# Kernel tuning notes

Hardware: AMD Instinct MI355X
Metric: run time of the kernel (lower is better)

The kernel has to match this reference:

```python
import jax, jax.numpy as jnp
import numpy as np

N_ATOMS = 16384
N_EDGES = 65536
ATOM_DIM = 29
BOND_DIM = 8
UNITS = 64          # message_units / embed_dim
STEPS = 4
HEADS = 8
DENSE = 512
B_MOL = 256         # molecules
T_ATOMS = 64        # atoms per molecule (N_ATOMS = B_MOL * T_ATOMS)


def setup_inputs() -> dict:
    key = jax.random.key(0)
    ks = jax.random.split(key, 24)
    D = UNITS

    atom_features = jax.random.normal(ks[0], (N_ATOMS, ATOM_DIM), jnp.float32)
    bond_features = jax.random.normal(ks[1], (N_EDGES, BOND_DIM), jnp.float32)
    # edges within molecules
    mol = jax.random.randint(ks[2], (N_EDGES,), 0, B_MOL)
    a = jax.random.randint(ks[3], (N_EDGES,), 0, T_ATOMS)
    b = jax.random.randint(ks[4], (N_EDGES,), 0, T_ATOMS)
    pair_indices = jnp.stack([mol * T_ATOMS + a, mol * T_ATOMS + b], axis=1).astype(jnp.int32)
    molecule_indicator = (jnp.arange(N_ATOMS) // T_ATOMS).astype(jnp.int32)

    def xavier(k, shape, fan_in):
        return jax.random.normal(k, shape, jnp.float32) * (1.0 / np.sqrt(fan_in))

    params = dict(
        kernel=xavier(ks[5], (BOND_DIM, D * D), BOND_DIM),
        kernel_bias=jnp.zeros((D * D,), jnp.float32),
        gru_w_ih=xavier(ks[6], (3 * D, D), D),
        gru_w_hh=xavier(ks[7], (3 * D, D), D),
        gru_b_ih=jnp.zeros((3 * D,), jnp.float32),
        gru_b_hh=jnp.zeros((3 * D,), jnp.float32),
        in_proj_w=xavier(ks[8], (3 * D, D), D),
        in_proj_b=jnp.zeros((3 * D,), jnp.float32),
        out_proj_w=xavier(ks[9], (D, D), D),
        out_proj_b=jnp.zeros((D,), jnp.float32),
        ffn_w1=xavier(ks[10], (D, DENSE), D),
        ffn_b1=jnp.zeros((DENSE,), jnp.float32),
        ffn_w2=xavier(ks[11], (DENSE, D), DENSE),
        ffn_b2=jnp.zeros((D,), jnp.float32),
        ln1_g=jnp.ones((D,), jnp.float32),
        ln1_b=jnp.zeros((D,), jnp.float32),
        ln2_g=jnp.ones((D,), jnp.float32),
        ln2_b=jnp.zeros((D,), jnp.float32),
        d1_w=xavier(ks[12], (D, DENSE), D),
        d1_b=jnp.zeros((DENSE,), jnp.float32),
        d2_w=xavier(ks[13], (DENSE, 1), DENSE),
        d2_b=jnp.zeros((1,), jnp.float32),
    )
    return dict(atom_features=atom_features, bond_features=bond_features,
                pair_indices=pair_indices, molecule_indicator=molecule_indicator, **params)


def _layernorm(x, g, b, eps=1e-5):
    mu = x.mean(-1, keepdims=True)
    var = ((x - mu) ** 2).mean(-1, keepdims=True)
    return (x - mu) * jax.lax.rsqrt(var + eps) * g + b


def _forward(atom_features, bond_features, pair_indices, molecule_indicator,
             kernel, kernel_bias, gru_w_ih, gru_w_hh, gru_b_ih, gru_b_hh,
             in_proj_w, in_proj_b, out_proj_w, out_proj_b,
             ffn_w1, ffn_b1, ffn_w2, ffn_b2, ln1_g, ln1_b, ln2_g, ln2_b,
             d1_w, d1_b, d2_w, d2_b):
    D = UNITS
    n = atom_features.shape[0]
    # pad atom features to message_units
    h = jnp.pad(atom_features, ((0, 0), (0, D - atom_features.shape[1])))

    src = pair_indices[:, 0]
    dst = pair_indices[:, 1]
    # per-edge bond-conditioned transform matrices: [E, D, D]
    bond_mat = (bond_features @ kernel + kernel_bias).reshape(-1, D, D)

    for _ in range(STEPS):
        nbr = h[dst]                                      # gather [E, D]
        msg = jnp.einsum('eij,ej->ei', bond_mat, nbr)     # per-edge matvec
        agg = jax.ops.segment_sum(msg, src, num_segments=n)  # scatter-add [N, D]
        # GRUCell(input=agg, hidden=h)
        gi = agg @ gru_w_ih.T + gru_b_ih
        gh = h @ gru_w_hh.T + gru_b_hh
        i_r, i_z, i_n = jnp.split(gi, 3, axis=-1)
        h_r, h_z, h_n = jnp.split(gh, 3, axis=-1)
        r = jax.nn.sigmoid(i_r + h_r)
        z = jax.nn.sigmoid(i_z + h_z)
        nn_ = jnp.tanh(i_n + r * h_n)
        h = (1.0 - z) * nn_ + z * h

    # PartitionPadding: scatter atoms into [B_MOL, T_ATOMS, D] (indicator sorted, contiguous)
    starts = jnp.searchsorted(molecule_indicator, jnp.arange(B_MOL, dtype=molecule_indicator.dtype))
    pos = jnp.arange(n) - starts[molecule_indicator]
    x = jnp.zeros((B_MOL, T_ATOMS, D), h.dtype).at[molecule_indicator, pos].set(h)

    valid = jnp.any(x != 0, axis=-1)                      # [B, T] key-padding mask

    # multi-head self-attention
    qkv = x @ in_proj_w.T + in_proj_b                     # [B, T, 3D]
    q, k, v = jnp.split(qkv, 3, axis=-1)
    hd = D // HEADS
    q = q.reshape(B_MOL, T_ATOMS, HEADS, hd)
    k = k.reshape(B_MOL, T_ATOMS, HEADS, hd)
    v = v.reshape(B_MOL, T_ATOMS, HEADS, hd)
    scores = jnp.einsum('bqhd,bkhd->bhqk', q, k) / np.sqrt(hd)
    scores = jnp.where(valid[:, None, None, :], scores, -1e9)
    attn = jax.nn.softmax(scores, axis=-1)
    ao = jnp.einsum('bhqk,bkhd->bqhd', attn, v).reshape(B_MOL, T_ATOMS, D)
    ao = ao @ out_proj_w.T + out_proj_b

    y1 = _layernorm(x + ao, ln1_g, ln1_b)
    ffn = jax.nn.relu(y1 @ ffn_w1 + ffn_b1) @ ffn_w2 + ffn_b2
    y2 = _layernorm(y1 + ffn, ln2_g, ln2_b)
    pooled = y2.mean(axis=1)                              # [B, D]

    out = jax.nn.relu(pooled @ d1_w + d1_b)
    return jax.nn.sigmoid(out @ d2_w + d2_b)              # [B, 1]


def reference(atom_features, bond_features, pair_indices, molecule_indicator,
              kernel, kernel_bias, gru_w_ih, gru_w_hh, gru_b_ih, gru_b_hh,
              in_proj_w, in_proj_b, out_proj_w, out_proj_b,
              ffn_w1, ffn_b1, ffn_w2, ffn_b2, ln1_g, ln1_b, ln2_g, ln2_b,
              d1_w, d1_b, d2_w, d2_b):
    return _forward(atom_features, bond_features, pair_indices, molecule_indicator,
                    kernel, kernel_bias, gru_w_ih, gru_w_hh, gru_b_ih, gru_b_hh,
                    in_proj_w, in_proj_b, out_proj_w, out_proj_b,
                    ffn_w1, ffn_b1, ffn_w2, ffn_b2, ln1_g, ln1_b, ln2_g, ln2_b,
                    d1_w, d1_b, d2_w, d2_b)
```

## Files before the change

kernel.cpp:

```cpp
#include <hip/hip_runtime.h>
#include <hip/hip_bf16.h>
#include <math.h>

#define NA 16384
#define NE 65536
#define AD 29

typedef __attribute__((ext_vector_type(8))) short bfrag8;
typedef __attribute__((ext_vector_type(4))) float f32x4;

__device__ __forceinline__ float sigmoidf_(float x) { return 1.0f / (1.0f + expf(-x)); }
__device__ __forceinline__ unsigned short bf16bits(float x) {
  __hip_bfloat16 hb = __float2bfloat16(x);
  return *reinterpret_cast<unsigned short*>(&hb);
}
__device__ __forceinline__ float bf16val(unsigned short u) {
  unsigned int b = ((unsigned int)u) << 16;
  return __uint_as_float(b);
}

__global__ void k_init_h(const float* __restrict__ af, float* __restrict__ h,
                         int* __restrict__ count) {
  int idx = blockIdx.x * 256 + threadIdx.x;
  if (idx >= NA * 64) return;
  if (idx < NA) count[idx] = 0;
  int a = idx >> 6, d = idx & 63;
  h[idx] = (d < AD) ? af[a * AD + d] : 0.0f;
}

__global__ void k_prep_all(
    const float* __restrict__ kern, const float* __restrict__ kbias,
    const float* __restrict__ wih, const float* __restrict__ whh,
    const float* __restrict__ w1, const float* __restrict__ w2,
    const float* __restrict__ ipw, const float* __restrict__ opw,
    unsigned short* __restrict__ KrA,
    unsigned short* __restrict__ Wh, unsigned short* __restrict__ Wl,
    unsigned short* __restrict__ W1h, unsigned short* __restrict__ W1l,
    unsigned short* __restrict__ W2h, unsigned short* __restrict__ W2l,
    unsigned short* __restrict__ PQh, unsigned short* __restrict__ PQl,
    unsigned short* __restrict__ POh, unsigned short* __restrict__ POl) {
  int idx0 = blockIdx.x * 256 + threadIdx.x;
  if (idx0 < 36864) {
    int idx = idx0;
    int r = idx & 7;
    int lane = (idx >> 3) & 63;
    int tmp2 = idx >> 9;
    int ks = tmp2 % 18, w = tmp2 / 18;
    int i = w * 16 + (lane & 15);
    int kj = ks * 32 + ((lane >> 4) << 3) + r;
    int k9 = kj >> 6, j = kj & 63;
    float v = (k9 < 8) ? kern[k9 * 4096 + i * 64 + j] : kbias[i * 64 + j];
    KrA[idx] = bf16bits(v);
  } else if (idx0 < 61440) {
    int idx = idx0 - 36864;
    int r = idx & 7;
    int lane = (idx >> 3) & 63;
    int t2 = idx >> 9;
    int ks = t2 & 1;
    int t3 = t2 >> 1;
    int q = t3 % 6, w = t3 / 6;
    int s = q / 3, g = q % 3;
    int R = g * 64 + w * 16 + (lane & 15);
    int kk = ks * 32 + ((lane >> 4) << 3) + r;
    float v = (s == 0) ? wih[R * 64 + kk] : whh[R * 64 + kk];
    unsigned short hi = bf16bits(v);
    Wh[idx] = hi;
    Wl[idx] = bf16bits(v - bf16val(hi));
  } else if (idx0 < 126976) {
    int idx = idx0 - 61440;
    int r = idx & 7;
    int lane = (idx >> 3) & 63;
    int rest = (idx >> 9) & 63;
    if (idx < 32768) {
      int tile = rest >> 1, ks = rest & 1;
      int hid = tile * 16 + (lane & 15);
      int kk = ks * 32 + ((lane >> 4) << 3) + r;
      float v = w1[kk * 512 + hid];
      unsigned short hi = bf16bits(v);
      W1h[idx] = hi;
      W1l[idx] = bf16bits(v - bf16val(hi));
    } else {
      int i2 = idx - 32768;
      int tile = rest >> 4, ks = rest & 15;
      int outr = tile * 16 + (lane & 15);
      int kk = ks * 32 + ((lane >> 4) << 3) + r;
      float v = w2[kk * 64 + outr];
      unsigned short hi = bf16bits(v);
      W2h[i2] = hi;
      W2l[i2] = bf16bits(v - bf16val(hi));
    }
  } else if (idx0 < 143360) {
    int i = idx0 - 126976;
    if (i < 12288) {
      int r = i & 7;
      int lane = (i >> 3) & 63;
      int rest = i >> 9;
      int t = rest >> 1, ks = rest & 1;
      int R = t * 16 + (lane & 15);
      int kk = ks * 32 + ((lane >> 4) << 3) + r;
      float v = ipw[R * 64 + kk];
      unsigned short hi = bf16bits(v);
      PQh[i] = hi;
      PQl[i] = bf16bits(v - bf16val(hi));
    } else {
      int i2 = i - 12288;
      int r = i2 & 7;
      int lane = (i2 >> 3) & 63;
      int rest = i2 >> 9;
      int t = rest >> 1, ks = rest & 1;
      int R = t * 16 + (lane & 15);
      int kk = ks * 32 + ((lane >> 4) << 3) + r;
      float v = opw[R * 64 + kk];
      unsigned short hi = bf16bits(v);
      POh[i2] = hi;
      POl[i2] = bf16bits(v - bf16val(hi));
    }
  }
}

__global__ void k_count(const int* __restrict__ pairs, int* __restrict__ count) {
  int e = blockIdx.x * 256 + threadIdx.x;
  if (e >= NE) return;
  atomicAdd(&count[pairs[2 * e]], 1);
}
__global__ void k_scan1(const int* __restrict__ count, int* __restrict__ bsum) {
  __shared__ int red[256];
  int b = blockIdx.x, t = threadIdx.x;
  red[t] = count[b * 256 + t];
  __syncthreads();
  for (int s = 128; s > 0; s >>= 1) { if (t < s) red[t] += red[t + s]; __syncthreads(); }
  if (t == 0) bsum[b] = red[0];
}
__global__ void k_scan2(const int* __restrict__ count, const int* __restrict__ bsum,
                        int* __restrict__ start, int* __restrict__ cursor) {
  __shared__ int sc[256];
  __shared__ int basev;
  int b = blockIdx.x, t = threadIdx.x;
  if (t == 0) { int s = 0; for (int i = 0; i < b; ++i) s += bsum[i]; basev = s; }
  int v = count[b * 256 + t];
  sc[t] = v;
  __syncthreads();
  for (int off = 1; off < 256; off <<= 1) {
    int add = (t >= off) ? sc[t - off] : 0;
    __syncthreads();
    sc[t] += add;
    __syncthreads();
  }
  int excl = sc[t] - v + basev;
  start[b * 256 + t] = excl;
  cursor[b * 256 + t] = excl;
  if (b * 256 + t == NA - 1) start[NA] = excl + v;
}
__global__ void k_place(const int* __restrict__ pairs, int* __restrict__ cursor,
                        int* __restrict__ elist) {
  int e = blockIdx.x * 256 + threadIdx.x;
  if (e >= NE) return;
  int pos = atomicAdd(&cursor[pairs[2 * e]], 1);
  elist[pos] = e;
}
__global__ void k_reorder(const float* __restrict__ bf, const int* __restrict__ pairs,
                          const int* __restrict__ elist, int* __restrict__ sdst,
                          float* __restrict__ sbf) {
  int idx = blockIdx.x * 256 + threadIdx.x;
  if (idx >= NE * 8) return;
  int pos = idx >> 3, k = idx & 7;
  int e = elist[pos];
  sbf[idx] = bf[e * 8 + k];
  if (k == 0) sdst[pos] = pairs[2 * e + 1];
}

#define MW 4
#define MAW 4
__global__ __launch_bounds__(256, 4) void k_msg(
    const float* __restrict__ h_in, const int* __restrict__ start,
    const int* __restrict__ sdst, const float* __restrict__ sbf,
    const unsigned short* __restrict__ KrA,
    const unsigned short* __restrict__ Wh, const unsigned short* __restrict__ Wl,
    const float* __restrict__ bih, const float* __restrict__ bhh,
    float* __restrict__ h_out) {
  __shared__ __align__(16) unsigned short Tb[16 * 584];
  __shared__ __align__(16) unsigned short Xh[16 * 136];
  __shared__ __align__(16) unsigned short Xl[16 * 136];
  __shared__ __align__(16) float Hf[16 * 68];
  __shared__ __align__(16) float AHa[16 * 68];
  __shared__ float bias_s[384];
  const int tid = threadIdx.x, lane = tid & 63, wv = tid >> 6;
  const int ablk = blockIdx.x * 16;
  const int awave = ablk + wv * MAW;

#pragma unroll
  for (int aa = 0; aa < MAW; ++aa) {
    const int a = wv * MAW + aa;
    const float v = h_in[(ablk + a) * 64 + lane];
    Hf[a * 68 + lane] = v;
    const unsigned short hi = bf16bits(v);
    Xh[a * 136 + 64 + lane] = hi;
    Xl[a * 136 + 64 + lane] = bf16bits(v - bf16val(hi));
  }
  if (tid < 192) { bias_s[tid] = bih[tid]; bias_s[192 + tid] = bhh[tid]; }

  for (int a = 0; a < MAW; ++a) {
    const int s0 = __builtin_amdgcn_readfirstlane(start[awave + a]);
    const int s1 = __builtin_amdgcn_readfirstlane(start[awave + a + 1]);
    float t[9] = {0.f, 0.f, 0.f, 0.f, 0.f, 0.f, 0.f, 0.f, 0.f};
    for (int base = s0; base < s1; base += 8) {
      const int nb = s1 - base;
      float hv[8];
#pragma unroll
      for (int i = 0; i < 8; ++i) {
        int d = (i < nb) ? sdst[base + i] : 0;
        hv[i] = (i < nb) ? h_in[d * 64 + lane] : 0.f;
      }
#pragma unroll
      for (int i = 0; i < 8; ++i) {
#pragma unroll
        for (int k = 0; k < 8; ++k)
          t[k] = fmaf(sbf[(base + i) * 8 + k], hv[i], t[k]);
        t[8] += hv[i];
      }
    }
    const int row = wv * MAW + a;
#pragma unroll
    for (int k = 0; k < 9; ++k) Tb[row * 584 + k * 64 + lane] = bf16bits(t[k]);
  }
  __syncthreads();

  f32x4 acc = {0.f, 0.f, 0.f, 0.f};
  const bfrag8* KrA8 = reinterpret_cast<const bfrag8*>(KrA);
  const int tb_base = (lane & 15) * 584 + ((lane >> 4) << 3);
#pragma unroll 3
  for (int ks = 0; ks < 18; ++ks) {
    bfrag8 af = KrA8[(wv * 18 + ks) * 64 + lane];
    bfrag8 bfr = *reinterpret_cast<const bfrag8*>(&Tb[tb_base + ks * 32]);
    acc = __builtin_amdgcn_mfma_f32_16x16x32_bf16(af, bfr, acc, 0, 0, 0);
  }
#pragma unroll
  for (int reg = 0; reg < 4; ++reg) {
    const int ii = wv * 16 + ((lane >> 4) << 2) + reg;
    const unsigned short hi = bf16bits(acc[reg]);
    Xh[(lane & 15) * 136 + ii] = hi;
    Xl[(lane & 15) * 136 + ii] = bf16bits(acc[reg] - bf16val(hi));
  }
  __syncthreads();

  const bfrag8* Wh8 = reinterpret_cast<const bfrag8*>(Wh);
  const bfrag8* Wl8 = reinterpret_cast<const bfrag8*>(Wl);
  f32x4 g0 = {0,0,0,0}, g1 = {0,0,0,0}, g2 = {0,0,0,0};
  f32x4 g3 = {0,0,0,0}, g4 = {0,0,0,0}, g5 = {0,0,0,0};
  f32x4* gptr[6] = {&g0, &g1, &g2, &g3, &g4, &g5};
#pragma unroll
  for (int q = 0; q < 6; ++q) {
    const int s = q / 3;
    f32x4 g = *gptr[q];
#pragma unroll
    for (int ks = 0; ks < 2; ++ks) {
      const int fidx = ((wv * 6 + q) * 2 + ks) * 64 + lane;
      bfrag8 Ah = Wh8[fidx];
      bfrag8 Al = Wl8[fidx];
      const int xoff = (lane & 15) * 136 + (s * 2 + ks) * 32 + ((lane >> 4) << 3);
      bfrag8 Bh = *reinterpret_cast<const bfrag8*>(&Xh[xoff]);
      bfrag8 Bl = *reinterpret_cast<const bfrag8*>(&Xl[xoff]);
      g = __builtin_amdgcn_mfma_f32_16x16x32_bf16(Ah, Bh, g, 0, 0, 0);
      g = __builtin_amdgcn_mfma_f32_16x16x32_bf16(Ah, Bl, g, 0, 0, 0);
      g = __builtin_amdgcn_mfma_f32_16x16x32_bf16(Al, Bh, g, 0, 0, 0);
    }
    *gptr[q] = g;
  }
#pragma unroll
  for (int reg = 0; reg < 4; ++reg) {
    const int i = wv * 16 + ((lane >> 4) << 2) + reg;
    const int atom = lane & 15;
    const float r = sigmoidf_(g0[reg] + bias_s[i] + g3[reg] + bias_s[192 + i]);
    const float z = sigmoidf_(g1[reg] + bias_s[64 + i] + g4[reg] + bias_s[256 + i]);
    const float nn = tanhf(g2[reg] + bias_s[128 + i] + r * (g5[reg] + bias_s[320 + i]));
    const float hold = Hf[atom * 68 + i];
    AHa[atom * 68 + i] = (1.0f - z) * nn + z * hold;
  }
  __syncthreads();
#pragma unroll
  for (int aa = 0; aa < MAW; ++aa) {
    const int a = wv * MAW + aa;
    h_out[(ablk + a) * 64 + lane] = AHa[a * 68 + lane];
  }
}

__global__ __launch_bounds__(256, 1) void k_mol(
    const float* __restrict__ h,
    const unsigned short* __restrict__ PQh, const unsigned short* __restrict__ PQl,
    const unsigned short* __restrict__ POh, const unsigned short* __restrict__ POl,
    const float* __restrict__ ipb, const float* __restrict__ opb,
    const float* __restrict__ l1g, const float* __restrict__ l1b,
    float* __restrict__ y1) {
  __shared__ __align__(16) float Hf[64 * 65];
  __shared__ __align__(16) unsigned short Xh[64 * 72];
  __shared__ __align__(16) unsigned short Xl[64 * 72];
  __shared__ __align__(16) float QKVs[192 * 65];
  __shared__ __align__(16) unsigned short AOh[64 * 72];
  __shared__ __align__(16) unsigned short AOl[64 * 72];
  __shared__ __align__(16) float Of[64 * 65];
  __shared__ int vd[64];
  const int tid = threadIdx.x, lane = tid & 63, wv = tid >> 6;
  const int mol = blockIdx.x;

  for (int aa = 0; aa < 16; ++aa) {
    const int a = wv * 16 + aa;
    const float v = h[(mol * 64 + a) * 64 + lane];
    Hf[a * 65 + lane] = v;
    const unsigned short hi = bf16bits(v);
    Xh[a * 72 + lane] = hi;
    Xl[a * 72 + lane] = bf16bits(v - bf16val(hi));
    int nz = __any(v != 0.0f);
    if (lane == 0) vd[a] = nz;
  }
  __syncthreads();

  const bfrag8* PQh8 = reinterpret_cast<const bfrag8*>(PQh);
  const bfrag8* PQl8 = reinterpret_cast<const bfrag8*>(PQl);
  const int xoff_b = (wv * 16 + (lane & 15)) * 72 + ((lane >> 4) << 3);
#pragma unroll 3
  for (int tile = 0; tile < 12; ++tile) {
    f32x4 acc = {0.f, 0.f, 0.f, 0.f};
#pragma unroll
    for (int ks = 0; ks < 2; ++ks) {
      const int fidx = (tile * 2 + ks) * 64 + lane;
      bfrag8 Ah = PQh8[fidx];
      bfrag8 Al = PQl8[fidx];
      bfrag8 Bh = *reinterpret_cast<const bfrag8*>(&Xh[xoff_b + ks * 32]);
      bfrag8 Bl = *reinterpret_cast<const bfrag8*>(&Xl[xoff_b + ks * 32]);
      acc = __builtin_amdgcn_mfma_f32_16x16x32_bf16(Ah, Bh, acc, 0, 0, 0);
      acc = __builtin_amdgcn_mfma_f32_16x16x32_bf16(Ah, Bl, acc, 0, 0, 0);
      acc = __builtin_amdgcn_mfma_f32_16x16x32_bf16(Al, Bh, acc, 0, 0, 0);
    }
#pragma unroll
    for (int reg = 0; reg < 4; ++reg) {
      const int row = tile * 16 + ((lane >> 4) << 2) + reg;
      QKVs[row * 65 + wv * 16 + (lane & 15)] = acc[reg] + ipb[row];
    }
  }
  __syncthreads();

#pragma unroll
  for (int hp = 0; hp < 2; ++hp) {
    const int hh = wv * 2 + hp;
    float q[8];
#pragma unroll
    for (int j = 0; j < 8; ++j) q[j] = QKVs[(hh * 8 + j) * 65 + lane];
    float m = -3.0e38f, l = 0.f, o[8] = {0,0,0,0,0,0,0,0};
    for (int t = 0; t < 64; ++t) {
      float s = 0.f;
#pragma unroll
      for (int j = 0; j < 8; ++j) s += q[j] * QKVs[(64 + hh * 8 + j) * 65 + t];
      s *= 0.35355339059327373f;
      s = vd[t] ? s : -1.0e9f;
      float mn = fmaxf(m, s);
      float c = expf(m - mn);
      float p = expf(s - mn);
      l = l * c + p;
#pragma unroll
      for (int j = 0; j < 8; ++j) o[j] = o[j] * c + p * QKVs[(128 + hh * 8 + j) * 65 + t];
      m = mn;
    }
    const float inv = 1.0f / l;
#pragma unroll
    for (int j = 0; j < 8; ++j) {
      const float v = o[j] * inv;
      const unsigned short hi = bf16bits(v);
      AOh[lane * 72 + hh * 8 + j] = hi;
      AOl[lane * 72 + hh * 8 + j] = bf16bits(v - bf16val(hi));
    }
  }
  __syncthreads();

  const bfrag8* POh8 = reinterpret_cast<const bfrag8*>(POh);
  const bfrag8* POl8 = reinterpret_cast<const bfrag8*>(POl);
  const int aoff_b = (wv * 16 + (lane & 15)) * 72 + ((lane >> 4) << 3);
#pragma unroll
  for (int tile = 0; tile < 4; ++tile) {
    f32x4 acc = {0.f, 0.f, 0.f, 0.f};
#pragma unroll
    for (int ks = 0; ks < 2; ++ks) {
      const int fidx = (tile * 2 + ks) * 64 + lane;
      bfrag8 Ah = POh8[fidx];
      bfrag8 Al = POl8[fidx];
      bfrag8 Bh = *reinterpret_cast<const bfrag8*>(&AOh[aoff_b + ks * 32]);
      bfrag8 Bl = *reinterpret_cast<const bfrag8*>(&AOl[aoff_b + ks * 32]);
      acc = __builtin_amdgcn_mfma_f32_16x16x32_bf16(Ah, Bh, acc, 0, 0, 0);
      acc = __builtin_amdgcn_mfma_f32_16x16x32_bf16(Ah, Bl, acc, 0, 0, 0);
      acc = __builtin_amdgcn_mfma_f32_16x16x32_bf16(Al, Bh, acc, 0, 0, 0);
    }
#pragma unroll
    for (int reg = 0; reg < 4; ++reg) {
      const int dim = tile * 16 + ((lane >> 4) << 2) + reg;
      Of[(wv * 16 + (lane & 15)) * 65 + dim] = acc[reg] + opb[dim];
    }
  }
  __syncthreads();

  const float gg = l1g[lane], bbb = l1b[lane];
  for (int aa = 0; aa < 16; ++aa) {
    const int a = wv * 16 + aa;
    float val = Hf[a * 65 + lane] + Of[a * 65 + lane];
    float s1 = val, s2 = val * val;
#pragma unroll
    for (int mm = 1; mm < 64; mm <<= 1) {
      s1 += __shfl_xor(s1, mm, 64);
      s2 += __shfl_xor(s2, mm, 64);
    }
    float mu = s1 * 0.015625f;
    float var = s2 * 0.015625f - mu * mu;
    y1[(mol * 64 + a) * 64 + lane] = (val - mu) * rsqrtf(var + 1e-5f) * gg + bbb;
  }
}

__global__ __launch_bounds__(256, 3) void k_ffn(
    const float* __restrict__ y1,
    const unsigned short* __restrict__ W1h, const unsigned short* __restrict__ W1l,
    const unsigned short* __restrict__ W2h, const unsigned short* __restrict__ W2l,
    const float* __restrict__ b1, const float* __restrict__ b2,
    const float* __restrict__ g, const float* __restrict__ bb,
    float* __restrict__ y2) {
  __shared__ __align__(16) unsigned short Xh[16 * 72];
  __shared__ __align__(16) unsigned short Xl[16 * 72];
  __shared__ __align__(16) unsigned short Hh[16 * 520];
  __shared__ __align__(16) unsigned short Hl[16 * 520];
  __shared__ __align__(16) float Y1f[16 * 68];
  __shared__ __align__(16) float Of[16 * 68];
  const int tid = threadIdx.x, lane = tid & 63, wv = tid >> 6;
  const int ablk = blockIdx.x * 16;

#pragma unroll
  for (int aa = 0; aa < 4; ++aa) {
    const int a = wv * 4 + aa;
    const float v = y1[(ablk + a) * 64 + lane];
    Y1f[a * 68 + lane] = v;
    const unsigned short hi = bf16bits(v);
    Xh[a * 72 + lane] = hi;
    Xl[a * 72 + lane] = bf16bits(v - bf16val(hi));
  }
  __syncthreads();

  const bfrag8* W1h8 = reinterpret_cast<const bfrag8*>(W1h);
  const bfrag8* W1l8 = reinterpret_cast<const bfrag8*>(W1l);
  const int xoff_base = (lane & 15) * 72 + ((lane >> 4) << 3);
#pragma unroll 2
  for (int t = 0; t < 8; ++t) {
    f32x4 acc = {0.f, 0.f, 0.f, 0.f};
    const int tile = wv * 8 + t;
#pragma unroll
    for (int ks = 0; ks < 2; ++ks) {
      const int fidx = (tile * 2 + ks) * 64 + lane;
      bfrag8 Ah = W1h8[fidx];
      bfrag8 Al = W1l8[fidx];
      bfrag8 Bh = *reinterpret_cast<const bfrag8*>(&Xh[xoff_base + ks * 32]);
      bfrag8 Bl = *reinterpret_cast<const bfrag8*>(&Xl[xoff_base + ks * 32]);
      acc = __builtin_amdgcn_mfma_f32_16x16x32_bf16(Ah, Bh, acc, 0, 0, 0);
      acc = __builtin_amdgcn_mfma_f32_16x16x32_bf16(Ah, Bl, acc, 0, 0, 0);
      acc = __builtin_amdgcn_mfma_f32_16x16x32_bf16(Al, Bh, acc, 0, 0, 0);
    }
#pragma unroll
    for (int reg = 0; reg < 4; ++reg) {
      const int hid = tile * 16 + ((lane >> 4) << 2) + reg;
      float val = fmaxf(acc[reg] + b1[hid], 0.f);
      const unsigned short hi = bf16bits(val);
      Hh[(lane & 15) * 520 + hid] = hi;
      Hl[(lane & 15) * 520 + hid] = bf16bits(val - bf16val(hi));
    }
  }
  __syncthreads();

  const bfrag8* W2h8 = reinterpret_cast<const bfrag8*>(W2h);
  const bfrag8* W2l8 = reinterpret_cast<const bfrag8*>(W2l);
  f32x4 acc2 = {0.f, 0.f, 0.f, 0.f};
  const int hoff_base = (lane & 15) * 520 + ((lane >> 4) << 3);
#pragma unroll 4
  for (int ks = 0; ks < 16; ++ks) {
    const int fidx = (wv * 16 + ks) * 64 + lane;
    bfrag8 Ah = W2h8[fidx];
    bfrag8 Al = W2l8[fidx];
    bfrag8 Bh = *reinterpret_cast<const bfrag8*>(&Hh[hoff_base + ks * 32]);
    bfrag8 Bl = *reinterpret_cast<const bfrag8*>(&Hl[hoff_base + ks * 32]);
    acc2 = __builtin_amdgcn_mfma_f32_16x16x32_bf16(Ah, Bh, acc2, 0, 0, 0);
    acc2 = __builtin_amdgcn_mfma_f32_16x16x32_bf16(Ah, Bl, acc2, 0, 0, 0);
    acc2 = __builtin_amdgcn_mfma_f32_16x16x32_bf16(Al, Bh, acc2, 0, 0, 0);
  }
#pragma unroll
  for (int reg = 0; reg < 4; ++reg) {
    const int outr = wv * 16 + ((lane >> 4) << 2) + reg;
    Of[(lane & 15) * 68 + outr] = acc2[reg] + b2[outr];
  }
  __syncthreads();

  const float gg = g[lane], bbb = bb[lane];
#pragma unroll
  for (int aa = 0; aa < 4; ++aa) {
    const int a = wv * 4 + aa;
    float val = Y1f[a * 68 + lane] + Of[a * 68 + lane];
    float s1 = val, s2 = val * val;
#pragma unroll
    for (int mm = 1; mm < 64; mm <<= 1) {
      s1 += __shfl_xor(s1, mm, 64);
      s2 += __shfl_xor(s2, mm, 64);
    }
    float mu = s1 * 0.015625f;
    float var = s2 * 0.015625f - mu * mu;
    y2[(ablk + a) * 64 + lane] = (val - mu) * rsqrtf(var + 1e-5f) * gg + bbb;
  }
}

__global__ __launch_bounds__(256) void k_head(
    const float* __restrict__ y2, const float* __restrict__ d1w,
    const float* __restrict__ d1b, const float* __restrict__ d2w,
    const float* __restrict__ d2b, float* __restrict__ out) {
  const int b = blockIdx.x;
  const int tid = threadIdx.x, lane = tid & 63, wv = tid >> 6;
  __shared__ float part[4][64];
  __shared__ float p_s[64];
  __shared__ float red_s[4];
  float s = 0.f;
#pragma unroll 4
  for (int t = wv * 16; t < wv * 16 + 16; ++t) s += y2[(b * 64 + t) * 64 + lane];
  part[wv][lane] = s;
  __syncthreads();
  if (tid < 64)
    p_s[tid] = (part[0][tid] + part[1][tid] + part[2][tid] + part[3][tid]) * 0.015625f;
  __syncthreads();
  float acc = 0.f;
#pragma unroll
  for (int rep = 0; rep < 2; ++rep) {
    int c = rep * 256 + tid;
    float hvv = d1b[c];
    for (int d = 0; d < 64; ++d) hvv += p_s[d] * d1w[d * 512 + c];
    acc += fmaxf(hvv, 0.f) * d2w[c];
  }
#pragma unroll
  for (int mm = 1; mm < 64; mm <<= 1) acc += __shfl_xor(acc, mm, 64);
  if ((tid & 63) == 0) red_s[tid >> 6] = acc;
  __syncthreads();
  if (tid == 0) {
    float t = red_s[0] + red_s[1] + red_s[2] + red_s[3] + d2b[0];
    out[b] = 1.0f / (1.0f + expf(-t));
  }
}

extern "C" void kernel_launch(void* const* d_in, const int* in_sizes, int n_in,
                              void* d_out, int out_size, void* d_ws, size_t ws_size,
                              hipStream_t stream) {
  (void)in_sizes; (void)n_in; (void)out_size; (void)ws_size;
  const float* af   = (const float*)d_in[0];
  const float* bfeat= (const float*)d_in[1];
  const int*   pairs= (const int*)d_in[2];
  const float* kern = (const float*)d_in[4];
  const float* kbias= (const float*)d_in[5];
  const float* wih  = (const float*)d_in[6];
  const float* whh  = (const float*)d_in[7];
  const float* bih  = (const float*)d_in[8];
  const float* bhh  = (const float*)d_in[9];
  const float* ipw  = (const float*)d_in[10];
  const float* ipb  = (const float*)d_in[11];
  const float* opw  = (const float*)d_in[12];
  const float* opb  = (const float*)d_in[13];
  const float* fw1  = (const float*)d_in[14];
  const float* fb1  = (const float*)d_in[15];
  const float* fw2  = (const float*)d_in[16];
  const float* fb2  = (const float*)d_in[17];
  const float* l1g  = (const float*)d_in[18];
  const float* l1b  = (const float*)d_in[19];
  const float* l2g  = (const float*)d_in[20];
  const float* l2b  = (const float*)d_in[21];
  const float* d1w  = (const float*)d_in[22];
  const float* d1b  = (const float*)d_in[23];
  const float* d2w  = (const float*)d_in[24];
  const float* d2b  = (const float*)d_in[25];
  float* out = (float*)d_out;

  float* ws = (float*)d_ws;
  float* h      = ws;
  float* h2     = h + (size_t)NA * 64;
  float* qkv    = h2 + (size_t)NA * 64;
  float* ao     = qkv + (size_t)NA * 192;
  float* y1     = ao + (size_t)NA * 64;
  float* y2     = y1 + (size_t)NA * 64;
  float* pooled = y2 + (size_t)NA * 64;
  int*   valid  = (int*)(pooled + 256 * 64);
  (void)ao; (void)pooled;

  unsigned short* W1h = (unsigned short*)(valid + NA);
  unsigned short* W1l = W1h + 32768;
  unsigned short* W2h = W1l + 32768;
  unsigned short* W2l = W2h + 32768;
  unsigned short* PQh = W2l + 32768;
  unsigned short* PQl = PQh + 12288;
  unsigned short* POh = PQl + 12288;
  unsigned short* POl = POh + 4096;

  unsigned short* KrA = (unsigned short*)qkv;
  int*   count  = (int*)(qkv + 36864);
  int*   start  = count + NA;
  int*   cursor = start + NA + 1;
  int*   elist  = cursor + NA;
  int*   bsum   = elist + NE;
  int*   sdst   = bsum + 256;
  float* sbf    = (float*)(sdst + NE + 8);
  unsigned short* Wh = (unsigned short*)(sbf + (size_t)NE * 8 + 64);
  unsigned short* Wl = Wh + 24576;

  k_init_h<<<NA * 64 / 256, 256, 0, stream>>>(af, h, count);
  k_prep_all<<<560, 256, 0, stream>>>(kern, kbias, wih, whh, fw1, fw2, ipw, opw,
                                      KrA, Wh, Wl, W1h, W1l, W2h, W2l,
                                      PQh, PQl, POh, POl);
  k_count<<<NE / 256, 256, 0, stream>>>(pairs, count);
  k_scan1<<<64, 256, 0, stream>>>(count, bsum);
  k_scan2<<<64, 256, 0, stream>>>(count, bsum, start, cursor);
  k_place<<<NE / 256, 256, 0, stream>>>(pairs, cursor, elist);
  k_reorder<<<NE * 8 / 256, 256, 0, stream>>>(bfeat, pairs, elist, sdst, sbf);

  float* hin = h;
  float* hout = h2;
  for (int s = 0; s < 4; ++s) {
    k_msg<<<NA / 16, 256, 0, stream>>>(hin, start, sdst, sbf, KrA,
                                       Wh, Wl, bih, bhh, hout);
    float* tmp = hin; hin = hout; hout = tmp;
  }

  k_mol<<<256, 256, 0, stream>>>(h, PQh, PQl, POh, POl, ipb, opb, l1g, l1b, y1);
  k_ffn<<<NA / 16, 256, 0, stream>>>(y1, W1h, W1l, W2h, W2l, fb1, fb2, l2g, l2b, y2);
  k_head<<<256, 256, 0, stream>>>(y2, d1w, d1b, d2w, d2b, out);
}
```

Measured before the change: 161.7 us.

## Fuse setup kernels and batch edge gathers across atoms in message kernel

Merges the h-initialisation kernel into the weight-prep kernel and folds the edge reorder into the placement kernel, so each edge's destination and bond features are written straight to their sorted slot and the intermediate edge list disappears. Two launches go away. In the message kernel, the first batch of up to eight neighbour gathers for all four atoms a wave handles is issued before any accumulation, giving more memory-level parallelism. The cost is higher register pressure from the per-atom accumulator and gather arrays.

```diff
diff --git a/kernel.cpp b/kernel.cpp
--- a/kernel.cpp
+++ b/kernel.cpp
@@ -19,16 +19,8 @@
   return __uint_as_float(b);
 }
 
-__global__ void k_init_h(const float* __restrict__ af, float* __restrict__ h,
-                         int* __restrict__ count) {
-  int idx = blockIdx.x * 256 + threadIdx.x;
-  if (idx >= NA * 64) return;
-  if (idx < NA) count[idx] = 0;
-  int a = idx >> 6, d = idx & 63;
-  h[idx] = (d < AD) ? af[a * AD + d] : 0.0f;
-}
-
-__global__ void k_prep_all(
+__global__ void k_init_prep(
+    const float* __restrict__ af, float* __restrict__ h, int* __restrict__ count,
     const float* __restrict__ kern, const float* __restrict__ kbias,
     const float* __restrict__ wih, const float* __restrict__ whh,
     const float* __restrict__ w1, const float* __restrict__ w2,
@@ -40,6 +32,12 @@
     unsigned short* __restrict__ PQh, unsigned short* __restrict__ PQl,
     unsigned short* __restrict__ POh, unsigned short* __restrict__ POl) {
   int idx0 = blockIdx.x * 256 + threadIdx.x;
+  if (idx0 >= NA * 64) return;
+  if (idx0 < NA) count[idx0] = 0;
+  {
+    int a = idx0 >> 6, d = idx0 & 63;
+    h[idx0] = (d < AD) ? af[a * AD + d] : 0.0f;
+  }
   if (idx0 < 36864) {
     int idx = idx0;
     int r = idx & 7;
@@ -152,21 +150,17 @@
   if (b * 256 + t == NA - 1) start[NA] = excl + v;
 }
 __global__ void k_place(const int* __restrict__ pairs, int* __restrict__ cursor,
-                        int* __restrict__ elist) {
+                        const float* __restrict__ bf, int* __restrict__ sdst,
+                        float* __restrict__ sbf) {
   int e = blockIdx.x * 256 + threadIdx.x;
   if (e >= NE) return;
-  int pos = atomicAdd(&cursor[pairs[2 * e]], 1);
-  elist[pos] = e;
-}
-__global__ void k_reorder(const float* __restrict__ bf, const int* __restrict__ pairs,
-                          const int* __restrict__ elist, int* __restrict__ sdst,
-                          float* __restrict__ sbf) {
-  int idx = blockIdx.x * 256 + threadIdx.x;
-  if (idx >= NE * 8) return;
-  int pos = idx >> 3, k = idx & 7;
-  int e = elist[pos];
-  sbf[idx] = bf[e * 8 + k];
-  if (k == 0) sdst[pos] = pairs[2 * e + 1];
+  int src = pairs[2 * e], dst = pairs[2 * e + 1];
+  int pos = atomicAdd(&cursor[src], 1);
+  sdst[pos] = dst;
+  const float4* b4 = reinterpret_cast<const float4*>(&bf[e * 8]);
+  float4* s4 = reinterpret_cast<float4*>(&sbf[(size_t)pos * 8]);
+  s4[0] = b4[0];
+  s4[1] = b4[1];
 }
 
 #define MW 4
@@ -199,29 +193,73 @@
   }
   if (tid < 192) { bias_s[tid] = bih[tid]; bias_s[192 + tid] = bhh[tid]; }
 
+  int s0[MAW], s1[MAW];
+#pragma unroll
   for (int a = 0; a < MAW; ++a) {
-    const int s0 = __builtin_amdgcn_readfirstlane(start[awave + a]);
-    const int s1 = __builtin_amdgcn_readfirstlane(start[awave + a + 1]);
-    float t[9] = {0.f, 0.f, 0.f, 0.f, 0.f, 0.f, 0.f, 0.f, 0.f};
-    for (int base = s0; base < s1; base += 8) {
-      const int nb = s1 - base;
-      float hv[8];
+    s0[a] = __builtin_amdgcn_readfirstlane(start[awave + a]);
+    s1[a] = __builtin_amdgcn_readfirstlane(start[awave + a + 1]);
+  }
+  float t[MAW][9];
+#pragma unroll
+  for (int a = 0; a < MAW; ++a)
+#pragma unroll
+    for (int k = 0; k < 9; ++k) t[a][k] = 0.f;
+
+  float hv[MAW][8];
+#pragma unroll
+  for (int a = 0; a < MAW; ++a) {
+    const int cnt = s1[a] - s0[a];
+#pragma unroll
+    for (int i = 0; i < 8; ++i) {
+      hv[a][i] = 0.f;
+      if (i < cnt) {
+        int d = sdst[s0[a] + i];
+        hv[a][i] = h_in[d * 64 + lane];
+      }
+    }
+  }
+#pragma unroll
+  for (int a = 0; a < MAW; ++a) {
+    const int cnt = s1[a] - s0[a];
+#pragma unroll
+    for (int i = 0; i < 8; ++i) {
+      if (i < cnt) {
+#pragma unroll
+        for (int k = 0; k < 8; ++k)
+          t[a][k] = fmaf(sbf[(size_t)(s0[a] + i) * 8 + k], hv[a][i], t[a][k]);
+        t[a][8] += hv[a][i];
+      }
+    }
+  }
+#pragma unroll
+  for (int a = 0; a < MAW; ++a) {
+    for (int base = s0[a] + 8; base < s1[a]; base += 8) {
+      const int nb = s1[a] - base;
+      float hv2[8];
 #pragma unroll
       for (int i = 0; i < 8; ++i) {
-        int d = (i < nb) ? sdst[base + i] : 0;
-        hv[i] = (i < nb) ? h_in[d * 64 + lane] : 0.f;
+        hv2[i] = 0.f;
+        if (i < nb) {
+          int d = sdst[base + i];
+          hv2[i] = h_in[d * 64 + lane];
+        }
       }
 #pragma unroll
       for (int i = 0; i < 8; ++i) {
-#pragma unroll
-        for (int k = 0; k < 8; ++k)
-          t[k] = fmaf(sbf[(base + i) * 8 + k], hv[i], t[k]);
-        t[8] += hv[i];
+        if (i < nb) {
+#pragma unroll
+          for (int k = 0; k < 8; ++k)
+            t[a][k] = fmaf(sbf[(size_t)(base + i) * 8 + k], hv2[i], t[a][k]);
+          t[a][8] += hv2[i];
+        }
       }
     }
+  }
+#pragma unroll
+  for (int a = 0; a < MAW; ++a) {
     const int row = wv * MAW + a;
 #pragma unroll
-    for (int k = 0; k < 9; ++k) Tb[row * 584 + k * 64 + lane] = bf16bits(t[k]);
+    for (int k = 0; k < 9; ++k) Tb[row * 584 + k * 64 + lane] = bf16bits(t[a][k]);
   }
   __syncthreads();
 
@@ -597,22 +635,19 @@
   int*   count  = (int*)(qkv + 36864);
   int*   start  = count + NA;
   int*   cursor = start + NA + 1;
-  int*   elist  = cursor + NA;
-  int*   bsum   = elist + NE;
+  int*   bsum   = cursor + NA;
   int*   sdst   = bsum + 256;
   float* sbf    = (float*)(sdst + NE + 8);
   unsigned short* Wh = (unsigned short*)(sbf + (size_t)NE * 8 + 64);
   unsigned short* Wl = Wh + 24576;
 
-  k_init_h<<<NA * 64 / 256, 256, 0, stream>>>(af, h, count);
-  k_prep_all<<<560, 256, 0, stream>>>(kern, kbias, wih, whh, fw1, fw2, ipw, opw,
-                                      KrA, Wh, Wl, W1h, W1l, W2h, W2l,
-                                      PQh, PQl, POh, POl);
+  k_init_prep<<<NA * 64 / 256, 256, 0, stream>>>(
+      af, h, count, kern, kbias, wih, whh, fw1, fw2, ipw, opw,
+      KrA, Wh, Wl, W1h, W1l, W2h, W2l, PQh, PQl, POh, POl);
   k_count<<<NE / 256, 256, 0, stream>>>(pairs, count);
   k_scan1<<<64, 256, 0, stream>>>(count, bsum);
   k_scan2<<<64, 256, 0, stream>>>(count, bsum, start, cursor);
-  k_place<<<NE / 256, 256, 0, stream>>>(pairs, cursor, elist);
-  k_reorder<<<NE * 8 / 256, 256, 0, stream>>>(bfeat, pairs, elist, sdst, sbf);
+  k_place<<<NE / 256, 256, 0, stream>>>(pairs, cursor, bfeat, sdst, sbf);
 
   float* hin = h;
   float* hout = h2;
```

Result: faster. 154.6 us (-4.4%).
